# Performance work log

Measured on AMD Instinct MI355X. Metric: run time of the kernel, lower is better.

Reference implementation:

```python
import jax, jax.numpy as jnp
import numpy as np

B, S, D, H, E, K = 4, 1024, 1024, 4096, 8, 2


def setup_inputs() -> dict:
    key = jax.random.key(0)
    ks = jax.random.split(key, 5)
    std = 0.02
    return {
        "x": jax.random.normal(ks[0], (B, S, D), dtype=jnp.float32),
        "router_W": jax.random.normal(ks[1], (D, E), dtype=jnp.float32) * std,
        "W_in": jax.random.normal(ks[2], (E, D, H), dtype=jnp.float32) * std,
        "b_in": jnp.zeros((E, H), dtype=jnp.float32),
        "W_out": jax.random.normal(ks[3], (E, H, D), dtype=jnp.float32) * std,
        "b_out": jnp.zeros((E, D), dtype=jnp.float32),
    }


def reference(x, router_W, W_in, b_in, W_out, b_out):
    # ---- routing ----
    logits = jnp.einsum("bsd,de->bse", x, router_W)          # [B,S,E]
    probs = jax.nn.softmax(logits, axis=-1)                    # [B,S,E]
    top_p, top_i = jax.lax.top_k(probs, K)                     # [B,S,K]
    top_p = top_p / (jnp.sum(top_p, axis=-1, keepdims=True) + 1e-8)
    one_hot = jax.nn.one_hot(top_i, E, dtype=x.dtype)          # [B,S,K,E]
    combine = jnp.sum(one_hot * top_p[..., None], axis=-2)     # [B,S,E] per-expert weight

    # ---- experts (original runs full batch through every selected expert;
    #      with E=8, K=2 all experts are active, so run all densely) ----
    h = jnp.einsum("bsd,edh->ebsh", x, W_in) + b_in[:, None, None, :]
    h = jax.nn.gelu(h, approximate=False)
    y = jnp.einsum("ebsh,ehd->ebsd", h, W_out) + b_out[:, None, None, :]
    out = jnp.einsum("bse,ebsd->bsd", combine, y)              # weighted combine

    # ---- load-balancing aux loss ----
    expert_usage = jnp.mean(one_hot, axis=(0, 1, 2))           # f_i, fraction of routed slots
    avg_probs = jnp.mean(probs, axis=(0, 1))                   # P_i
    aux_loss = E * jnp.sum(avg_probs * expert_usage)
    return out, aux_loss
```

## Files before the change

kernel.cpp:

```cpp
#include <hip/hip_runtime.h>
#include <hip/hip_bf16.h>
#include <math.h>

#define B_ 4
#define S_ 1024
#define T_ (B_ * S_)
#define D_ 1024
#define H_ 4096
#define E_ 8
#define K_ 2
#define A_ (T_ * K_)
#define NTM_ 40

typedef __bf16 bf16x8_t __attribute__((ext_vector_type(8)));
typedef float f32x4_t __attribute__((ext_vector_type(4)));
typedef unsigned short u16x8_t __attribute__((ext_vector_type(8)));

__device__ inline unsigned short f2bf(float f) {
    __hip_bfloat16 h = __float2bfloat16(f);
    return *reinterpret_cast<unsigned short*>(&h);
}

__device__ __forceinline__ float fast_gelu(float v) {
    float z = v * 0.70710678118654752440f;
    float az = fabsf(z);
    float t = __builtin_amdgcn_rcpf(1.0f + 0.3275911f * az);
    float poly = ((((1.061405429f * t - 1.453152027f) * t + 1.421413741f) * t
                   - 0.284496736f) * t + 0.254829592f) * t;
    float e = __expf(-az * az);
    float erfv = 1.0f - poly * e;
    erfv = (z < 0.0f) ? -erfv : erfv;
    return 0.5f * v * (1.0f + erfv);
}

__device__ __forceinline__ void gl2lds16(const unsigned short* g, unsigned short* l) {
    auto* gp = reinterpret_cast<const __attribute__((address_space(1))) unsigned int*>(
        reinterpret_cast<uintptr_t>(g));
    auto* lp = reinterpret_cast<__attribute__((address_space(3))) unsigned int*>(
        reinterpret_cast<uintptr_t>(l));
    __builtin_amdgcn_global_load_lds(gp, lp, 16, 0, 0);
}

__global__ void router_kernel(const float* __restrict__ x, const float* __restrict__ rw,
                              int* __restrict__ tok_e, float* __restrict__ tok_w,
                              int* __restrict__ counts_pad, float* __restrict__ probs_pad) {
    __shared__ float s_probs[E_];
    __shared__ int s_counts[E_];
    const int tid = threadIdx.x;
    if (tid < E_) { s_probs[tid] = 0.f; s_counts[tid] = 0; }
    __syncthreads();
    const int wave = tid >> 6;
    const int lane = tid & 63;

    float wprob[E_];
    int wcount[E_];
#pragma unroll
    for (int e = 0; e < E_; ++e) { wprob[e] = 0.f; wcount[e] = 0; }

    for (int tt = 0; tt < 4; ++tt) {
        const int token = blockIdx.x * 16 + wave * 4 + tt;
        const float* xr = x + (long)token * D_;
        float acc[E_];
#pragma unroll
        for (int e = 0; e < E_; ++e) acc[e] = 0.f;
        for (int i = 0; i < D_ / 64; ++i) {
            int d = i * 64 + lane;
            float xv = xr[d];
            const float* w = rw + (long)d * E_;
#pragma unroll
            for (int e = 0; e < E_; ++e) acc[e] += xv * w[e];
        }
#pragma unroll
        for (int e = 0; e < E_; ++e) {
            for (int off = 32; off > 0; off >>= 1)
                acc[e] += __shfl_down(acc[e], off);
        }
        if (lane == 0) {
            float m = acc[0];
            for (int e = 1; e < E_; ++e) m = fmaxf(m, acc[e]);
            float p[E_], s = 0.f;
            for (int e = 0; e < E_; ++e) { p[e] = expf(acc[e] - m); s += p[e]; }
            float inv = 1.f / s;
            for (int e = 0; e < E_; ++e) { p[e] *= inv; wprob[e] += p[e]; }
            int i0 = 0;
            for (int e = 1; e < E_; ++e) if (p[e] > p[i0]) i0 = e;
            int i1 = (i0 == 0) ? 1 : 0;
            for (int e = 0; e < E_; ++e) if (e != i0 && p[e] > p[i1]) i1 = e;
            float w0 = p[i0], w1 = p[i1];
            float inv2 = 1.f / (w0 + w1 + 1e-8f);
            tok_e[token * 2] = i0;
            tok_e[token * 2 + 1] = i1;
            tok_w[token * 2] = w0 * inv2;
            tok_w[token * 2 + 1] = w1 * inv2;
            wcount[i0]++; wcount[i1]++;
        }
    }
    if (lane == 0) {
#pragma unroll
        for (int e = 0; e < E_; ++e) {
            atomicAdd(&s_probs[e], wprob[e]);
            if (wcount[e]) atomicAdd(&s_counts[e], wcount[e]);
        }
    }
    __syncthreads();
    if (tid < E_) {
        atomicAdd(&probs_pad[tid * 32], s_probs[tid]);
        if (s_counts[tid]) atomicAdd(&counts_pad[tid * 32], s_counts[tid]);
    }
}

__global__ void offsets_aux_kernel(const int* __restrict__ counts_pad,
                                   const float* __restrict__ probs_pad,
                                   int* __restrict__ offsets,
                                   int* __restrict__ tile_e, int* __restrict__ tile_m,
                                   int* __restrict__ n_tiles, float* __restrict__ aux_out) {
    if (threadIdx.x == 0 && blockIdx.x == 0) {
        int run = 0, t = 0;
        for (int e = 0; e < E_; ++e) {
            int c = counts_pad[e * 32];
            offsets[e] = run;
            for (int m0 = 0; m0 < c; m0 += 256) {
                tile_e[t] = e; tile_m[t] = m0; ++t;
            }
            run += c;
        }
        offsets[E_] = run;
        *n_tiles = t;
        float aux = 0.f;
        for (int e = 0; e < E_; ++e)
            aux += (probs_pad[e * 32] / (float)T_) * ((float)counts_pad[e * 32] / (float)A_);
        *aux_out = (float)E_ * aux;
    }
}

__global__ void scatter_kernel(const int* __restrict__ tok_e, const float* __restrict__ tok_w,
                               const int* __restrict__ offsets, int* __restrict__ cursors_pad,
                               int* __restrict__ perm_token, float* __restrict__ perm_weight,
                               int* __restrict__ inv_pos) {
    int i = blockIdx.x * blockDim.x + threadIdx.x;
    int lane = threadIdx.x & 63;
    int e = tok_e[i];
    float w = tok_w[i];
    unsigned long long bal[E_];
#pragma unroll
    for (int q = 0; q < E_; ++q) bal[q] = __ballot(e == q);
    unsigned long long below = (1ull << lane) - 1ull;
    int rank = __popcll(bal[e] & below);
    int base = 0;
    if (lane < E_) {
        int c = __popcll(bal[lane]);
        if (c) base = atomicAdd(&cursors_pad[lane * 32], c);
    }
    int mybase = __shfl(base, e);
    int pos = offsets[e] + mybase + rank;
    perm_token[pos] = i >> 1;
    perm_weight[pos] = w;
    inv_pos[i] = pos;
}

__global__ void cast_x_kernel(const float* __restrict__ x, unsigned short* __restrict__ xb) {
    long i = (long)blockIdx.x * blockDim.x + threadIdx.x;
    float4 v = reinterpret_cast<const float4*>(x)[i];
    unsigned long long packed = (unsigned long long)f2bf(v.x)
        | ((unsigned long long)f2bf(v.y) << 16)
        | ((unsigned long long)f2bf(v.z) << 32)
        | ((unsigned long long)f2bf(v.w) << 48);
    reinterpret_cast<unsigned long long*>(xb)[i] = packed;
}

__global__ void transpose_cast_kernel(const float* __restrict__ in, unsigned short* __restrict__ out,
                                      int R, int C) {
    __shared__ float tile[64][65];
    const long e = blockIdx.z;
    const float* in_e = in + e * (long)R * C;
    unsigned short* out_e = out + e * (long)R * C;
    const int c0 = blockIdx.x * 64;
    const int r0 = blockIdx.y * 64;
    const int tid = threadIdx.x;
    const int c4 = (tid & 15) * 4;
    const int rb = tid >> 4;
#pragma unroll
    for (int i = 0; i < 4; ++i) {
        const int r = rb + i * 16;
        const float4 v = *reinterpret_cast<const float4*>(&in_e[(long)(r0 + r) * C + c0 + c4]);
        tile[r][c4] = v.x; tile[r][c4 + 1] = v.y; tile[r][c4 + 2] = v.z; tile[r][c4 + 3] = v.w;
    }
    __syncthreads();
    const int rs = (tid & 7) * 8;
    const int cb = tid >> 3;
#pragma unroll
    for (int i = 0; i < 2; ++i) {
        const int c = cb + i * 32;
        u16x8_t p;
#pragma unroll
        for (int j = 0; j < 8; ++j) p[j] = f2bf(tile[rs + j][c]);
        *reinterpret_cast<u16x8_t*>(&out_e[(long)(c0 + c) * R + r0 + rs]) = p;
    }
}

template <int PHASE, int NSPLIT>
__device__ __forceinline__ void gemm_body(const unsigned short* __restrict__ A_src,
                                const unsigned short* __restrict__ B_src,
                                const float* __restrict__ bias,
                                const int* __restrict__ offsets,
                                const int* __restrict__ tile_e, const int* __restrict__ tile_m,
                                const int* __restrict__ p_ntiles,
                                const int* __restrict__ perm_token,
                                const float* __restrict__ perm_weight,
                                unsigned short* __restrict__ h_buf,
                                float* __restrict__ y_perm) {
    constexpr int Ksz  = (PHASE == 1) ? D_ : H_;
    constexpr int Kloc = Ksz / NSPLIT;
    constexpr int Nsz  = (PHASE == 1) ? H_ : D_;
    constexpr int NT   = Kloc / 32;
    constexpr int NTN  = Nsz / 256;

    const int nwg = gridDim.x;
    const int id = blockIdx.x;
    const int q = nwg >> 3, r8 = nwg & 7;
    const int xcd = id & 7, sub = id >> 3;
    const int wg = (xcd < r8 ? xcd * (q + 1) : r8 * (q + 1) + (xcd - r8) * q) + sub;
    const int mt = wg % NTM_;
    if (mt >= *p_ntiles) return;
    const int rest = wg / NTM_;
    const int nt = rest % NTN;
    const int kh = rest / NTN;
    const int e = tile_e[mt];
    const int m0 = tile_m[mt];
    const int off_e = offsets[e];
    const int n_e = offsets[e + 1] - off_e;
    const int n0 = nt * 256;
    const long k_base = (long)kh * Kloc;

    __shared__ __attribute__((aligned(16))) unsigned short lds_a[4 * 8192];
    __shared__ __attribute__((aligned(16))) unsigned short lds_b[4 * 8192];

    const int tid = threadIdx.x;
    const int lane = tid & 63;
    const int wave = tid >> 6;
    const int wr = wave >> 2;
    const int wc = wave & 3;
    const int lrow = lane & 15;
    const int kg = lane >> 4;

    const int srow = lane >> 2;
    const int grow = wave * 16 + srow;
    const int sc = (lane & 3) ^ ((grow >> 1) & 3);
    const int m_loc = m0 + grow;
    const int m_cl = (m_loc < n_e) ? m_loc : (n_e - 1);
    const int spos = off_e + m_cl;
    long arow;
    if (PHASE == 1) arow = (long)perm_token[spos] * Ksz;
    else            arow = (long)spos * Ksz;
    const unsigned short* gA = A_src + arow + k_base + sc * 8;
    const unsigned short* gB = B_src + (long)e * Nsz * Ksz + (long)(n0 + grow) * Ksz + k_base + sc * 8;
    unsigned short* const la0 = lds_a + wave * 512;
    unsigned short* const lb0 = lds_b + wave * 512;

    int aoff[4], boff[4];
#pragma unroll
    for (int i = 0; i < 4; ++i) {
        const int r = wr * 64 + i * 16 + lrow;
        aoff[i] = r * 32 + ((kg ^ ((r >> 1) & 3)) * 8);
        const int c = wc * 64 + i * 16 + lrow;
        boff[i] = c * 32 + ((kg ^ ((c >> 1) & 3)) * 8);
    }

    f32x4_t acc[4][4];
#pragma unroll
    for (int i = 0; i < 4; ++i)
#pragma unroll
        for (int j = 0; j < 4; ++j) acc[i][j] = (f32x4_t){0.f, 0.f, 0.f, 0.f};

#pragma unroll
    for (int tt = 0; tt < 3; ++tt) {
        gl2lds16(gA + tt * 32, la0 + tt * 8192);
        gl2lds16(gB + tt * 32, lb0 + tt * 8192);
    }

    for (int t = 0; t < NT; ++t) {
        if (t + 2 < NT)      asm volatile("s_waitcnt vmcnt(4)" ::: "memory");
        else if (t + 1 < NT) asm volatile("s_waitcnt vmcnt(2)" ::: "memory");
        else                 asm volatile("s_waitcnt vmcnt(0)" ::: "memory");
        __builtin_amdgcn_s_barrier();
        if (t + 3 < NT) {
            gl2lds16(gA + (t + 3) * 32, la0 + ((t + 3) & 3) * 8192);
            gl2lds16(gB + (t + 3) * 32, lb0 + ((t + 3) & 3) * 8192);
        }
        const unsigned short* la = lds_a + (t & 3) * 8192;
        const unsigned short* lb = lds_b + (t & 3) * 8192;
        bf16x8_t af[4], bf[4];
#pragma unroll
        for (int i = 0; i < 4; ++i) {
            af[i] = *reinterpret_cast<const bf16x8_t*>(la + aoff[i]);
            bf[i] = *reinterpret_cast<const bf16x8_t*>(lb + boff[i]);
        }
        asm volatile("s_waitcnt lgkmcnt(0)" ::: "memory");
        __builtin_amdgcn_sched_barrier(0);
        __builtin_amdgcn_s_setprio(1);
#pragma unroll
        for (int i = 0; i < 4; ++i)
#pragma unroll
            for (int j = 0; j < 4; ++j)
                acc[i][j] = __builtin_amdgcn_mfma_f32_16x16x32_bf16(af[i], bf[j], acc[i][j], 0, 0, 0);
        __builtin_amdgcn_s_setprio(0);
    }

    const float* bias_e = bias + (long)e * Nsz;
#pragma unroll
    for (int i = 0; i < 4; ++i) {
#pragma unroll
        for (int rq = 0; rq < 4; ++rq) {
            const int row_loc = wr * 64 + i * 16 + kg * 4 + rq;
            const int m_out = m0 + row_loc;
            if (m_out >= n_e) continue;
            const int pos = off_e + m_out;
            if (PHASE == 1) {
#pragma unroll
                for (int j = 0; j < 4; ++j) {
                    const int n = n0 + wc * 64 + j * 16 + lrow;
                    float v = acc[i][j][rq] + bias_e[n];
                    h_buf[(long)pos * Nsz + n] = f2bf(fast_gelu(v));
                }
            } else {
                float* yp = y_perm + (long)kh * ((long)A_ * D_);
                const float wgt = perm_weight[pos];
#pragma unroll
                for (int j = 0; j < 4; ++j) {
                    const int n = n0 + wc * 64 + j * 16 + lrow;
                    float v = acc[i][j][rq] + ((kh == 0) ? bias_e[n] : 0.f);
                    yp[(long)pos * Nsz + n] = v * wgt;
                }
            }
        }
    }
}

#define GEMM_ARGS const unsigned short* __restrict__ A_src, \
                  const unsigned short* __restrict__ B_src, \
                  const float* __restrict__ bias, \
                  const int* __restrict__ offsets, \
                  const int* __restrict__ tile_e, const int* __restrict__ tile_m, \
                  const int* __restrict__ p_ntiles, \
                  const int* __restrict__ perm_token, \
                  const float* __restrict__ perm_weight, \
                  unsigned short* __restrict__ h_buf, \
                  float* __restrict__ y_perm
#define GEMM_PASS A_src, B_src, bias, offsets, tile_e, tile_m, p_ntiles, \
                  perm_token, perm_weight, h_buf, y_perm

__launch_bounds__(1024, 4)
__global__ void moe_gemm_p1(GEMM_ARGS) { gemm_body<1, 1>(GEMM_PASS); }
__launch_bounds__(1024, 4)
__global__ void moe_gemm_p2s1(GEMM_ARGS) { gemm_body<2, 1>(GEMM_PASS); }
__launch_bounds__(1024, 4)
__global__ void moe_gemm_p2s2(GEMM_ARGS) { gemm_body<2, 2>(GEMM_PASS); }
__launch_bounds__(1024, 4)
__global__ void moe_gemm_p2s4(GEMM_ARGS) { gemm_body<2, 4>(GEMM_PASS); }

__global__ void combine_kernel(const float* __restrict__ y_perm, const int* __restrict__ inv_pos,
                               float* __restrict__ out, int ns) {
    int t = blockIdx.x;
    int d4 = threadIdx.x;
    int p0 = inv_pos[t * 2];
    int p1 = inv_pos[t * 2 + 1];
    float4 o = {0.f, 0.f, 0.f, 0.f};
    for (int s = 0; s < ns; ++s) {
        const float4* y = reinterpret_cast<const float4*>(y_perm + (long)s * A_ * D_);
        float4 a = y[(long)p0 * (D_ / 4) + d4];
        float4 b = y[(long)p1 * (D_ / 4) + d4];
        o.x += a.x + b.x; o.y += a.y + b.y; o.z += a.z + b.z; o.w += a.w + b.w;
    }
    reinterpret_cast<float4*>(out + (long)t * D_)[d4] = o;
}

extern "C" void kernel_launch(void* const* d_in, const int* in_sizes, int n_in,
                              void* d_out, int out_size, void* d_ws, size_t ws_size,
                              hipStream_t stream) {
    const float* x        = (const float*)d_in[0];
    const float* router_W = (const float*)d_in[1];
    const float* W_in     = (const float*)d_in[2];
    const float* b_in     = (const float*)d_in[3];
    const float* W_out    = (const float*)d_in[4];
    const float* b_out    = (const float*)d_in[5];
    float* out = (float*)d_out;

    char* ws = (char*)d_ws;
    size_t off = 0;
    auto alloc = [&](size_t bytes) -> void* {
        void* p = ws + off;
        off += (bytes + 255) & ~(size_t)255;
        return p;
    };

    int ns = 1;
    if (ws_size >= (size_t)340 * 1024 * 1024)      ns = 4;
    else if (ws_size >= (size_t)272 * 1024 * 1024) ns = 2;

    char* ctrl = (char*)alloc(4096);
    int* counts_pad   = (int*)ctrl;
    float* probs_pad  = (float*)(ctrl + 1024);
    int* cursors_pad  = (int*)(ctrl + 2048);
    int* offsets      = (int*)(ctrl + 3072);
    int* tile_e       = (int*)(ctrl + 3200);
    int* tile_m       = (int*)(ctrl + 3584);
    int* n_tiles      = (int*)(ctrl + 3968);
    int* tok_e         = (int*)alloc((size_t)A_ * 4);
    float* tok_w       = (float*)alloc((size_t)A_ * 4);
    int* perm_token    = (int*)alloc((size_t)A_ * 4);
    float* perm_weight = (float*)alloc((size_t)A_ * 4);
    int* inv_pos       = (int*)alloc((size_t)A_ * 4);
    unsigned short* x_bf    = (unsigned short*)alloc((size_t)T_ * D_ * 2);
    unsigned short* w_in_t  = (unsigned short*)alloc((size_t)E_ * D_ * H_ * 2);
    unsigned short* w_out_t = (unsigned short*)alloc((size_t)E_ * D_ * H_ * 2);
    unsigned short* h_buf   = (unsigned short*)alloc((size_t)A_ * H_ * 2);
    float* y_perm           = (float*)alloc((size_t)ns * A_ * D_ * 4);

    hipMemsetAsync(ctrl, 0, 4096, stream);

    cast_x_kernel<<<(T_ * D_ / 4) / 256, 256, 0, stream>>>(x, x_bf);
    transpose_cast_kernel<<<dim3(H_ / 64, D_ / 64, E_), 256, 0, stream>>>(W_in, w_in_t, D_, H_);
    transpose_cast_kernel<<<dim3(D_ / 64, H_ / 64, E_), 256, 0, stream>>>(W_out, w_out_t, H_, D_);
    router_kernel<<<T_ / 16, 256, 0, stream>>>(x, router_W, tok_e, tok_w, counts_pad, probs_pad);
    offsets_aux_kernel<<<1, 64, 0, stream>>>(counts_pad, probs_pad, offsets,
                                             tile_e, tile_m, n_tiles, out + (out_size - 1));
    scatter_kernel<<<A_ / 256, 256, 0, stream>>>(tok_e, tok_w, offsets, cursors_pad,
                                                 perm_token, perm_weight, inv_pos);

    moe_gemm_p1<<<NTM_ * (H_ / 256), 1024, 0, stream>>>(
        x_bf, w_in_t, b_in, offsets, tile_e, tile_m, n_tiles,
        perm_token, perm_weight, h_buf, y_perm);
    if (ns == 4) {
        moe_gemm_p2s4<<<NTM_ * (D_ / 256) * 4, 1024, 0, stream>>>(
            h_buf, w_out_t, b_out, offsets, tile_e, tile_m, n_tiles,
            perm_token, perm_weight, h_buf, y_perm);
    } else if (ns == 2) {
        moe_gemm_p2s2<<<NTM_ * (D_ / 256) * 2, 1024, 0, stream>>>(
            h_buf, w_out_t, b_out, offsets, tile_e, tile_m, n_tiles,
            perm_token, perm_weight, h_buf, y_perm);
    } else {
        moe_gemm_p2s1<<<NTM_ * (D_ / 256), 1024, 0, stream>>>(
            h_buf, w_out_t, b_out, offsets, tile_e, tile_m, n_tiles,
            perm_token, perm_weight, h_buf, y_perm);
    }
    combine_kernel<<<T_, 256, 0, stream>>>(y_perm, inv_pos, out, ns);
}
```

Before: 634.9 us.

## Restructure MoE GEMM to 512 threads with 8x4 MFMA tiles and interleaved LDS pipeline

The expert GEMM kernels drop from 16 waves to 8 waves per 256x256 tile. Each wave now computes 128x64 outputs instead of 64x64, which raises register reuse of the A/B fragments. The K loop moves to 64-wide steps, double-buffered in LDS as four 32-wide sub-stages, with global-to-LDS prefetches for the next step interleaved between MFMA groups. This is meant to overlap loads with compute and cut per-FLOP LDS reads. In exchange it uses far more registers, which lowers occupancy, and adds extra barriers per step.

```diff
diff --git a/kernel.cpp b/kernel.cpp
--- a/kernel.cpp
+++ b/kernel.cpp
@@ -212,7 +212,7 @@
     constexpr int Ksz  = (PHASE == 1) ? D_ : H_;
     constexpr int Kloc = Ksz / NSPLIT;
     constexpr int Nsz  = (PHASE == 1) ? H_ : D_;
-    constexpr int NT   = Kloc / 32;
+    constexpr int NT   = Kloc / 64;
     constexpr int NTN  = Nsz / 256;
 
     const int nwg = gridDim.x;
@@ -232,8 +232,8 @@
     const int n0 = nt * 256;
     const long k_base = (long)kh * Kloc;
 
-    __shared__ __attribute__((aligned(16))) unsigned short lds_a[4 * 8192];
-    __shared__ __attribute__((aligned(16))) unsigned short lds_b[4 * 8192];
+    __shared__ __attribute__((aligned(16))) unsigned short lds_a[32768];
+    __shared__ __attribute__((aligned(16))) unsigned short lds_b[32768];
 
     const int tid = threadIdx.x;
     const int lane = tid & 63;
@@ -243,75 +243,160 @@
     const int lrow = lane & 15;
     const int kg = lane >> 4;
 
-    const int srow = lane >> 2;
-    const int grow = wave * 16 + srow;
-    const int sc = (lane & 3) ^ ((grow >> 1) & 3);
-    const int m_loc = m0 + grow;
-    const int m_cl = (m_loc < n_e) ? m_loc : (n_e - 1);
-    const int spos = off_e + m_cl;
-    long arow;
-    if (PHASE == 1) arow = (long)perm_token[spos] * Ksz;
-    else            arow = (long)spos * Ksz;
-    const unsigned short* gA = A_src + arow + k_base + sc * 8;
-    const unsigned short* gB = B_src + (long)e * Nsz * Ksz + (long)(n0 + grow) * Ksz + k_base + sc * 8;
-    unsigned short* const la0 = lds_a + wave * 512;
-    unsigned short* const lb0 = lds_b + wave * 512;
-
-    int aoff[4], boff[4];
-#pragma unroll
-    for (int i = 0; i < 4; ++i) {
-        const int r = wr * 64 + i * 16 + lrow;
-        aoff[i] = r * 32 + ((kg ^ ((r >> 1) & 3)) * 8);
-        const int c = wc * 64 + i * 16 + lrow;
-        boff[i] = c * 32 + ((kg ^ ((c >> 1) & 3)) * 8);
-    }
-
-    f32x4_t acc[4][4];
-#pragma unroll
-    for (int i = 0; i < 4; ++i)
+    const int sc = (lane & 3) ^ ((lane >> 3) & 3);
+    const unsigned short* gA[2];
+    const unsigned short* gB[2];
+    int st_off[2];
+#pragma unroll
+    for (int j = 0; j < 2; ++j) {
+        const int rr = (j * 8 + wave) * 16 + (lane >> 2);
+        const int m_loc = m0 + rr;
+        const int m_cl = (m_loc < n_e) ? m_loc : (n_e - 1);
+        const int pos = off_e + m_cl;
+        long arow;
+        if (PHASE == 1) arow = (long)perm_token[pos] * Ksz;
+        else            arow = (long)pos * Ksz;
+        gA[j] = A_src + arow + k_base + sc * 8;
+        gB[j] = B_src + (long)e * Nsz * Ksz + (long)(n0 + rr) * Ksz + k_base + sc * 8;
+        st_off[j] = (j * 8 + wave) * 512;
+    }
+
+    const int rch = (kg ^ ((lrow >> 1) & 3)) * 8;
+    const int a_rd = (wr * 128 + lrow) * 32 + rch;
+    const int b_rd = (wc * 64 + lrow) * 32 + rch;
+
+    f32x4_t acc[8][4];
+#pragma unroll
+    for (int i = 0; i < 8; ++i)
 #pragma unroll
         for (int j = 0; j < 4; ++j) acc[i][j] = (f32x4_t){0.f, 0.f, 0.f, 0.f};
 
-#pragma unroll
-    for (int tt = 0; tt < 3; ++tt) {
-        gl2lds16(gA + tt * 32, la0 + tt * 8192);
-        gl2lds16(gB + tt * 32, lb0 + tt * 8192);
-    }
+    bf16x8_t a0[8], a1[8], b0[4], b1[4];
+
+    gl2lds16(gA[0], lds_a + st_off[0]);
+    gl2lds16(gA[1], lds_a + st_off[1]);
+    gl2lds16(gB[0], lds_b + st_off[0]);
+    gl2lds16(gB[1], lds_b + st_off[1]);
+    gl2lds16(gA[0] + 32, lds_a + 8192 + st_off[0]);
+    gl2lds16(gA[1] + 32, lds_a + 8192 + st_off[1]);
+    gl2lds16(gB[0] + 32, lds_b + 8192 + st_off[0]);
+    gl2lds16(gB[1] + 32, lds_b + 8192 + st_off[1]);
 
     for (int t = 0; t < NT; ++t) {
-        if (t + 2 < NT)      asm volatile("s_waitcnt vmcnt(4)" ::: "memory");
-        else if (t + 1 < NT) asm volatile("s_waitcnt vmcnt(2)" ::: "memory");
-        else                 asm volatile("s_waitcnt vmcnt(0)" ::: "memory");
-        __builtin_amdgcn_s_barrier();
-        if (t + 3 < NT) {
-            gl2lds16(gA + (t + 3) * 32, la0 + ((t + 3) & 3) * 8192);
-            gl2lds16(gB + (t + 3) * 32, lb0 + ((t + 3) & 3) * 8192);
-        }
-        const unsigned short* la = lds_a + (t & 3) * 8192;
-        const unsigned short* lb = lds_b + (t & 3) * 8192;
-        bf16x8_t af[4], bf[4];
-#pragma unroll
-        for (int i = 0; i < 4; ++i) {
-            af[i] = *reinterpret_cast<const bf16x8_t*>(la + aoff[i]);
-            bf[i] = *reinterpret_cast<const bf16x8_t*>(lb + boff[i]);
-        }
+        const int cur = (t & 1) << 14;
+        const int nxt = 16384 - cur;
+        const int toff = (t + 1) * 64;
+        const bool pf = (t + 1 < NT);
+
+        asm volatile("s_waitcnt vmcnt(6)" ::: "memory");
+        __builtin_amdgcn_s_barrier();
+        asm volatile("" ::: "memory");
+#pragma unroll
+        for (int i = 0; i < 8; ++i)
+            a0[i] = *reinterpret_cast<const bf16x8_t*>(lds_a + cur + a_rd + i * 512);
+        if (pf) {
+            gl2lds16(gA[0] + toff, lds_a + nxt + st_off[0]);
+            gl2lds16(gA[1] + toff, lds_a + nxt + st_off[1]);
+        }
+        __builtin_amdgcn_s_barrier();
+        asm volatile("s_waitcnt lgkmcnt(0)" ::: "memory");
+        __builtin_amdgcn_sched_barrier(0);
+        if (t > 0) {
+            __builtin_amdgcn_s_setprio(1);
+#pragma unroll
+            for (int f = 0; f < 4; ++f)
+#pragma unroll
+                for (int j = 0; j < 4; ++j)
+                    acc[4 + f][j] = __builtin_amdgcn_mfma_f32_16x16x32_bf16(
+                        a1[4 + f], b1[j], acc[4 + f][j], 0, 0, 0);
+            __builtin_amdgcn_s_setprio(0);
+        }
+
+        if (pf) asm volatile("s_waitcnt vmcnt(6)" ::: "memory");
+        else    asm volatile("s_waitcnt vmcnt(4)" ::: "memory");
+        __builtin_amdgcn_s_barrier();
+        asm volatile("" ::: "memory");
+#pragma unroll
+        for (int j = 0; j < 4; ++j)
+            b0[j] = *reinterpret_cast<const bf16x8_t*>(lds_b + cur + b_rd + j * 512);
+        if (pf) {
+            gl2lds16(gB[0] + toff, lds_b + nxt + st_off[0]);
+            gl2lds16(gB[1] + toff, lds_b + nxt + st_off[1]);
+        }
+        __builtin_amdgcn_s_barrier();
         asm volatile("s_waitcnt lgkmcnt(0)" ::: "memory");
         __builtin_amdgcn_sched_barrier(0);
         __builtin_amdgcn_s_setprio(1);
 #pragma unroll
-        for (int i = 0; i < 4; ++i)
+        for (int f = 0; f < 4; ++f)
 #pragma unroll
             for (int j = 0; j < 4; ++j)
-                acc[i][j] = __builtin_amdgcn_mfma_f32_16x16x32_bf16(af[i], bf[j], acc[i][j], 0, 0, 0);
+                acc[f][j] = __builtin_amdgcn_mfma_f32_16x16x32_bf16(
+                    a0[f], b0[j], acc[f][j], 0, 0, 0);
         __builtin_amdgcn_s_setprio(0);
-    }
+
+        if (pf) asm volatile("s_waitcnt vmcnt(6)" ::: "memory");
+        else    asm volatile("s_waitcnt vmcnt(2)" ::: "memory");
+        __builtin_amdgcn_s_barrier();
+        asm volatile("" ::: "memory");
+#pragma unroll
+        for (int i = 0; i < 8; ++i)
+            a1[i] = *reinterpret_cast<const bf16x8_t*>(lds_a + cur + 8192 + a_rd + i * 512);
+        if (pf) {
+            gl2lds16(gA[0] + toff + 32, lds_a + nxt + 8192 + st_off[0]);
+            gl2lds16(gA[1] + toff + 32, lds_a + nxt + 8192 + st_off[1]);
+        }
+        __builtin_amdgcn_s_barrier();
+        asm volatile("s_waitcnt lgkmcnt(0)" ::: "memory");
+        __builtin_amdgcn_sched_barrier(0);
+        __builtin_amdgcn_s_setprio(1);
+#pragma unroll
+        for (int f = 0; f < 4; ++f)
+#pragma unroll
+            for (int j = 0; j < 4; ++j)
+                acc[4 + f][j] = __builtin_amdgcn_mfma_f32_16x16x32_bf16(
+                    a0[4 + f], b0[j], acc[4 + f][j], 0, 0, 0);
+        __builtin_amdgcn_s_setprio(0);
+
+        if (pf) asm volatile("s_waitcnt vmcnt(6)" ::: "memory");
+        else    asm volatile("s_waitcnt vmcnt(0)" ::: "memory");
+        __builtin_amdgcn_s_barrier();
+        asm volatile("" ::: "memory");
+#pragma unroll
+        for (int j = 0; j < 4; ++j)
+            b1[j] = *reinterpret_cast<const bf16x8_t*>(lds_b + cur + 8192 + b_rd + j * 512);
+        if (pf) {
+            gl2lds16(gB[0] + toff + 32, lds_b + nxt + 8192 + st_off[0]);
+            gl2lds16(gB[1] + toff + 32, lds_b + nxt + 8192 + st_off[1]);
+        }
+        __builtin_amdgcn_s_barrier();
+        asm volatile("s_waitcnt lgkmcnt(0)" ::: "memory");
+        __builtin_amdgcn_sched_barrier(0);
+        __builtin_amdgcn_s_setprio(1);
+#pragma unroll
+        for (int f = 0; f < 4; ++f)
+#pragma unroll
+            for (int j = 0; j < 4; ++j)
+                acc[f][j] = __builtin_amdgcn_mfma_f32_16x16x32_bf16(
+                    a1[f], b1[j], acc[f][j], 0, 0, 0);
+        __builtin_amdgcn_s_setprio(0);
+    }
+
+    __builtin_amdgcn_s_setprio(1);
+#pragma unroll
+    for (int f = 0; f < 4; ++f)
+#pragma unroll
+        for (int j = 0; j < 4; ++j)
+            acc[4 + f][j] = __builtin_amdgcn_mfma_f32_16x16x32_bf16(
+                a1[4 + f], b1[j], acc[4 + f][j], 0, 0, 0);
+    __builtin_amdgcn_s_setprio(0);
 
     const float* bias_e = bias + (long)e * Nsz;
 #pragma unroll
-    for (int i = 0; i < 4; ++i) {
+    for (int i = 0; i < 8; ++i) {
 #pragma unroll
         for (int rq = 0; rq < 4; ++rq) {
-            const int row_loc = wr * 64 + i * 16 + kg * 4 + rq;
+            const int row_loc = wr * 128 + i * 16 + kg * 4 + rq;
             const int m_out = m0 + row_loc;
             if (m_out >= n_e) continue;
             const int pos = off_e + m_out;
@@ -349,13 +434,13 @@
 #define GEMM_PASS A_src, B_src, bias, offsets, tile_e, tile_m, p_ntiles, \
                   perm_token, perm_weight, h_buf, y_perm
 
-__launch_bounds__(1024, 4)
+__launch_bounds__(512, 2)
 __global__ void moe_gemm_p1(GEMM_ARGS) { gemm_body<1, 1>(GEMM_PASS); }
-__launch_bounds__(1024, 4)
+__launch_bounds__(512, 2)
 __global__ void moe_gemm_p2s1(GEMM_ARGS) { gemm_body<2, 1>(GEMM_PASS); }
-__launch_bounds__(1024, 4)
+__launch_bounds__(512, 2)
 __global__ void moe_gemm_p2s2(GEMM_ARGS) { gemm_body<2, 2>(GEMM_PASS); }
-__launch_bounds__(1024, 4)
+__launch_bounds__(512, 2)
 __global__ void moe_gemm_p2s4(GEMM_ARGS) { gemm_body<2, 4>(GEMM_PASS); }
 
 __global__ void combine_kernel(const float* __restrict__ y_perm, const int* __restrict__ inv_pos,
@@ -427,19 +512,19 @@
     scatter_kernel<<<A_ / 256, 256, 0, stream>>>(tok_e, tok_w, offsets, cursors_pad,
                                                  perm_token, perm_weight, inv_pos);
 
-    moe_gemm_p1<<<NTM_ * (H_ / 256), 1024, 0, stream>>>(
+    moe_gemm_p1<<<NTM_ * (H_ / 256), 512, 0, stream>>>(
         x_bf, w_in_t, b_in, offsets, tile_e, tile_m, n_tiles,
         perm_token, perm_weight, h_buf, y_perm);
     if (ns == 4) {
-        moe_gemm_p2s4<<<NTM_ * (D_ / 256) * 4, 1024, 0, stream>>>(
+        moe_gemm_p2s4<<<NTM_ * (D_ / 256) * 4, 512, 0, stream>>>(
             h_buf, w_out_t, b_out, offsets, tile_e, tile_m, n_tiles,
             perm_token, perm_weight, h_buf, y_perm);
     } else if (ns == 2) {
-        moe_gemm_p2s2<<<NTM_ * (D_ / 256) * 2, 1024, 0, stream>>>(
+        moe_gemm_p2s2<<<NTM_ * (D_ / 256) * 2, 512, 0, stream>>>(
             h_buf, w_out_t, b_out, offsets, tile_e, tile_m, n_tiles,
             perm_token, perm_weight, h_buf, y_perm);
     } else {
-        moe_gemm_p2s1<<<NTM_ * (D_ / 256), 1024, 0, stream>>>(
+        moe_gemm_p2s1<<<NTM_ * (D_ / 256), 512, 0, stream>>>(
             h_buf, w_out_t, b_out, offsets, tile_e, tile_m, n_tiles,
             perm_token, perm_weight, h_buf, y_perm);
     }
```

Result: slower. 664.9 us (+4.7%).
